# Kernel optimization log

Measured on AMD Instinct MI355X. Metric: run time of the kernel, lower is better.

The kernel has to match this reference:

```python
import jax, jax.numpy as jnp
import numpy as np

N_HEADS = 32
N_KV_HEADS = 8
HEAD_DIM = 64
ROPE_BASE = 10000.0


def _rope(t):
    # t: [b, s, h, d]; Llama-style rotate-half RoPE
    b, s, h, d = t.shape
    inv_freq = 1.0 / (ROPE_BASE ** (jnp.arange(0, d, 2, dtype=jnp.float32) / d))
    freqs = jnp.arange(s, dtype=jnp.float32)[:, None] * inv_freq[None, :]  # [s, d/2]
    cos = jnp.cos(freqs)[None, :, None, :].astype(t.dtype)
    sin = jnp.sin(freqs)[None, :, None, :].astype(t.dtype)
    t1, t2 = t[..., : d // 2], t[..., d // 2 :]
    return jnp.concatenate([t1 * cos - t2 * sin, t2 * cos + t1 * sin], axis=-1)


def setup_inputs() -> dict:
    key = jax.random.key(0)
    ks = jax.random.split(key, 5)
    b, s, d = 2, 2048, 2048
    dkv = d // (N_HEADS // N_KV_HEADS)
    sc = 1.0 / np.sqrt(d)
    return {
        "x": jax.random.normal(ks[0], (b, s, d), jnp.float32),
        "wq": jax.random.normal(ks[1], (d, d), jnp.float32) * sc,
        "wk": jax.random.normal(ks[2], (d, dkv), jnp.float32) * sc,
        "wv": jax.random.normal(ks[3], (d, dkv), jnp.float32) * sc,
        "wo": jax.random.normal(ks[4], (d, d), jnp.float32) * sc,
    }


def reference(x, wq, wk, wv, wo):
    b, s, d = x.shape
    g = N_HEADS // N_KV_HEADS
    q = (x @ wq).reshape(b, s, N_HEADS, HEAD_DIM)
    k = (x @ wk).reshape(b, s, N_KV_HEADS, HEAD_DIM)
    v = (x @ wv).reshape(b, s, N_KV_HEADS, HEAD_DIM)
    q = _rope(q)
    k = _rope(k)
    # GQA: repeat kv heads to match query heads
    k = jnp.repeat(k, g, axis=2)  # [b, s, N_HEADS, d_h]
    v = jnp.repeat(v, g, axis=2)
    scale = 1.0 / np.sqrt(HEAD_DIM)
    scores = jnp.einsum("bqhd,bkhd->bhqk", q, k) * scale  # [b, h, s, s]
    causal = jnp.tril(jnp.ones((s, s), dtype=bool))
    scores = jnp.where(causal[None, None], scores, jnp.finfo(scores.dtype).min)
    probs = jax.nn.softmax(scores, axis=-1)
    out = jnp.einsum("bhqk,bkhd->bqhd", probs, v).reshape(b, s, d)
    return out @ wo
```

## Files before the change

### kernel.cpp

```cpp
#include <hip/hip_runtime.h>
#include <hip/hip_bf16.h>
#include <stdint.h>

typedef __attribute__((ext_vector_type(8))) __bf16 bf16x8;
typedef __attribute__((ext_vector_type(4))) __bf16 bf16x4;
typedef __attribute__((ext_vector_type(4))) float f32x4;

#define QSCALE (0.125f * 1.44269504f)

#define GL16(src, dst) __builtin_amdgcn_global_load_lds( \
    (const __attribute__((address_space(1))) void*)(src), \
    (__attribute__((address_space(3))) void*)(dst), 16, 0, 0)

static __device__ inline unsigned pkbf(float a, float b) {
  __bf16 x = (__bf16)a, y = (__bf16)b;
  unsigned short ux = __builtin_bit_cast(unsigned short, x);
  unsigned short uy = __builtin_bit_cast(unsigned short, y);
  return ((unsigned)uy << 16) | ux;
}

static __device__ inline float ex2(float x) {
#if __has_builtin(__builtin_amdgcn_exp2f)
  return __builtin_amdgcn_exp2f(x);
#else
  float r;
  asm("v_exp_f32 %0, %1" : "=v"(r) : "v"(x));
  return r;
#endif
}

__global__ void k_cvt(const float* __restrict__ in, __bf16* __restrict__ out, int n8) {
  int i = blockIdx.x * blockDim.x + threadIdx.x;
  if (i >= n8) return;
  const float4* p = (const float4*)(in) + (size_t)i * 2;
  float4 a = p[0], b = p[1];
  bf16x8 o;
  o[0] = (__bf16)a.x; o[1] = (__bf16)a.y; o[2] = (__bf16)a.z; o[3] = (__bf16)a.w;
  o[4] = (__bf16)b.x; o[5] = (__bf16)b.y; o[6] = (__bf16)b.z; o[7] = (__bf16)b.w;
  ((bf16x8*)out)[i] = o;
}

__global__ void k_tconv(const float* __restrict__ w, __bf16* __restrict__ wT, int K, int N) {
  __shared__ float tile[32][33];
  int n0 = blockIdx.x * 32, k0 = blockIdx.y * 32;
  int tx = threadIdx.x, ty = threadIdx.y;
#pragma unroll
  for (int i = 0; i < 32; i += 8)
    tile[ty + i][tx] = w[(size_t)(k0 + ty + i) * N + n0 + tx];
  __syncthreads();
#pragma unroll
  for (int i = 0; i < 32; i += 8)
    wT[(size_t)(n0 + ty + i) * K + k0 + tx] = (__bf16)tile[tx][ty + i];
}

__global__ void k_ropetab(float* __restrict__ ct, float* __restrict__ st) {
  int i = blockIdx.x * blockDim.x + threadIdx.x;
  if (i >= 2048 * 32) return;
  int s = i >> 5, j = i & 31;
  float invf = powf(10000.0f, -(float)j / 32.0f);
  float fr = (float)s * invf;
  ct[i] = cosf(fr);
  st[i] = sinf(fr);
}

template <int BN, int NW, int WPN, int MODE>
__global__ __launch_bounds__(NW * 64, NW / 4) void k_gemm256(const __bf16* __restrict__ A,
                                                             const __bf16* __restrict__ BT,
                                                             void* __restrict__ C0,
                                                             __bf16* __restrict__ kb,
                                                             __bf16* __restrict__ vt,
                                                             const float* __restrict__ ct,
                                                             const float* __restrict__ st,
                                                             int K, int NBN) {
  constexpr int WPM = NW / WPN;
  constexpr int MF = 256 / WPM / 16;
  constexpr int NF = BN / WPN / 16;
  constexpr int MH = MF / 2;
  constexpr int CHA = 256 * 8;
  constexpr int CHB = BN * 8;
  constexpr int PA = CHA / (NW * 64);
  constexpr int RA = CHA - PA * NW * 64;
  constexpr int PB = CHB / (NW * 64);
  static_assert(CHB % (NW * 64) == 0, "B chunks must tile threads");
  static_assert(RA % 64 == 0, "A remainder must be wave-aligned");
  static_assert(NF == 4, "epilogue assumes 64-col wave window");
  __shared__ __align__(16) __bf16 lA[2][256 * 64];
  __shared__ __align__(16) __bf16 lB[2][BN * 64];
  int bm = (blockIdx.x / NBN) << 8;
  int bn = (blockIdx.x % NBN) * BN;
  int tid = threadIdx.x, l = tid & 63, w = tid >> 6;
  int wr = w / WPN, wc = w % WPN;
  int lrow = l & 15, lk = l >> 4;
  int NT = K >> 6;
  f32x4 acc[MF][NF] = {};

#define STG(T, BUF)                                                           \
  do {                                                                        \
    int k0_ = (T) << 6;                                                       \
    _Pragma("unroll") for (int i_ = 0; i_ < PA; i_++) {                       \
      int ch_ = i_ * (NW * 64) + tid;                                         \
      int r_ = ch_ >> 3, c_ = ch_ & 7;                                        \
      GL16(A + (size_t)(bm + r_) * K + k0_ + ((c_ ^ (r_ & 7)) << 3),          \
           &lA[BUF][(i_ * (NW * 64) + (w << 6)) * 8]);                        \
    }                                                                         \
    if constexpr (RA > 0) {                                                   \
      if (tid < RA) {                                                         \
        int ch_ = PA * (NW * 64) + tid;                                       \
        int r_ = ch_ >> 3, c_ = ch_ & 7;                                      \
        GL16(A + (size_t)(bm + r_) * K + k0_ + ((c_ ^ (r_ & 7)) << 3),        \
             &lA[BUF][(PA * (NW * 64) + (w << 6)) * 8]);                      \
      }                                                                       \
    }                                                                         \
    _Pragma("unroll") for (int i_ = 0; i_ < PB; i_++) {                       \
      int ch_ = i_ * (NW * 64) + tid;                                         \
      int r_ = ch_ >> 3, c_ = ch_ & 7;                                        \
      GL16(BT + (size_t)(bn + r_) * K + k0_ + ((c_ ^ (r_ & 7)) << 3),         \
           &lB[BUF][(i_ * (NW * 64) + (w << 6)) * 8]);                        \
    }                                                                         \
  } while (0)

#define WAITN()                                                               \
  do {                                                                        \
    if constexpr (RA > 0) {                                                   \
      if (w < (RA >> 6))                                                      \
        asm volatile("s_waitcnt vmcnt(%0)" ::"i"(PA + PB + 1) : "memory");    \
      else                                                                    \
        asm volatile("s_waitcnt vmcnt(%0)" ::"i"(PA + PB) : "memory");        \
    } else {                                                                  \
      asm volatile("s_waitcnt vmcnt(%0)" ::"i"(PA + PB) : "memory");          \
    }                                                                         \
  } while (0)

  STG(0, 0);
  STG(1, 1);
  WAITN();
  __builtin_amdgcn_sched_barrier(0);
  __builtin_amdgcn_s_barrier();

  for (int t = 0; t < NT; t++) {
    int buf = t & 1;
    const char* bA = (const char*)lA[buf];
    const char* bB = (const char*)lB[buf];
    bf16x8 bfr[NF][2], af0[MH][2], af1[MH][2];
#pragma unroll
    for (int nf = 0; nf < NF; nf++) {
      int row = wc * (NF * 16) + nf * 16 + lrow;
#pragma unroll
      for (int kc = 0; kc < 2; kc++)
        bfr[nf][kc] = *(const bf16x8*)(bB + row * 128 +
                                       ((kc * 64 + 16 * lk) ^ ((row & 7) << 4)));
    }
#pragma unroll
    for (int mf = 0; mf < MH; mf++) {
      int row = wr * (MF * 16) + mf * 16 + lrow;
#pragma unroll
      for (int kc = 0; kc < 2; kc++)
        af0[mf][kc] = *(const bf16x8*)(bA + row * 128 +
                                       ((kc * 64 + 16 * lk) ^ ((row & 7) << 4)));
    }
    __builtin_amdgcn_s_setprio(1);
#pragma unroll
    for (int kc = 0; kc < 2; kc++)
#pragma unroll
      for (int mf = 0; mf < MH; mf++)
#pragma unroll
        for (int nf = 0; nf < NF; nf++)
          acc[mf][nf] = __builtin_amdgcn_mfma_f32_16x16x32_bf16(af0[mf][kc], bfr[nf][kc],
                                                                acc[mf][nf], 0, 0, 0);
    __builtin_amdgcn_s_setprio(0);
#pragma unroll
    for (int mf = 0; mf < MH; mf++) {
      int row = wr * (MF * 16) + (MH + mf) * 16 + lrow;
#pragma unroll
      for (int kc = 0; kc < 2; kc++)
        af1[mf][kc] = *(const bf16x8*)(bA + row * 128 +
                                       ((kc * 64 + 16 * lk) ^ ((row & 7) << 4)));
    }
    asm volatile("s_waitcnt lgkmcnt(0)" ::: "memory");
    __builtin_amdgcn_sched_barrier(0);
    __builtin_amdgcn_s_barrier();
    if (t + 2 < NT) STG(t + 2, buf);
    __builtin_amdgcn_s_setprio(1);
#pragma unroll
    for (int kc = 0; kc < 2; kc++)
#pragma unroll
      for (int mf = 0; mf < MH; mf++)
#pragma unroll
        for (int nf = 0; nf < NF; nf++)
          acc[MH + mf][nf] = __builtin_amdgcn_mfma_f32_16x16x32_bf16(
              af1[mf][kc], bfr[nf][kc], acc[MH + mf][nf], 0, 0, 0);
    __builtin_amdgcn_s_setprio(0);
    if (t + 2 < NT) {
      WAITN();
    } else {
      asm volatile("s_waitcnt vmcnt(0)" ::: "memory");
    }
    __builtin_amdgcn_sched_barrier(0);
    __builtin_amdgcn_s_barrier();
  }
#undef STG
#undef WAITN

  if constexpr (MODE == 0) {
    int wcb = bn + wc * 64;
    __bf16* qb = (__bf16*)C0;
    if (wcb < 2048) {
#pragma unroll
      for (int mf = 0; mf < MF; mf++)
#pragma unroll
        for (int r = 0; r < 4; r++) {
          int row = bm + wr * (MF * 16) + mf * 16 + 4 * lk + r;
          int sidx = row & 2047;
#pragma unroll
          for (int nfl = 0; nfl < 2; nfl++) {
            int d = nfl * 16 + lrow;
            float c = ct[sidx * 32 + d], sn = st[sidx * 32 + d];
            float a = acc[mf][nfl][r], b2 = acc[mf][nfl + 2][r];
            qb[(size_t)row * 2048 + wcb + d] = (__bf16)((a * c - b2 * sn) * QSCALE);
            qb[(size_t)row * 2048 + wcb + d + 32] = (__bf16)((b2 * c + a * sn) * QSCALE);
          }
        }
    } else if (wcb < 2560) {
      int cb = wcb - 2048;
#pragma unroll
      for (int mf = 0; mf < MF; mf++)
#pragma unroll
        for (int r = 0; r < 4; r++) {
          int row = bm + wr * (MF * 16) + mf * 16 + 4 * lk + r;
          int sidx = row & 2047;
#pragma unroll
          for (int nfl = 0; nfl < 2; nfl++) {
            int d = nfl * 16 + lrow;
            float c = ct[sidx * 32 + d], sn = st[sidx * 32 + d];
            float a = acc[mf][nfl][r], b2 = acc[mf][nfl + 2][r];
            kb[(size_t)row * 512 + cb + d] = (__bf16)(a * c - b2 * sn);
            kb[(size_t)row * 512 + cb + d + 32] = (__bf16)(b2 * c + a * sn);
          }
        }
    } else {
      int hkk = (wcb - 2560) >> 6;
#pragma unroll
      for (int mf = 0; mf < MF; mf++)
#pragma unroll
        for (int nf = 0; nf < NF; nf++)
#pragma unroll
          for (int r = 0; r < 4; r++) {
            int row = bm + wr * (MF * 16) + mf * 16 + 4 * lk + r;
            int dd = nf * 16 + lrow;
            int bb = row >> 11, s = row & 2047;
            vt[(size_t)(((bb << 3) + hkk) * 64 + dd) * 2048 + s] = (__bf16)acc[mf][nf][r];
          }
    }
  } else {
    float* C = (float*)C0;
#pragma unroll
    for (int mf = 0; mf < MF; mf++)
#pragma unroll
      for (int nf = 0; nf < NF; nf++)
#pragma unroll
        for (int r = 0; r < 4; r++) {
          int row = bm + wr * (MF * 16) + mf * 16 + 4 * lk + r;
          int col = bn + wc * 64 + nf * 16 + lrow;
          C[(size_t)row * 2048 + col] = acc[mf][nf][r];
        }
  }
}

template <int BN, int NW, int WPN, int MODE>
__global__ __launch_bounds__(NW * 64, NW / 4) void k_gemm3d(const __bf16* __restrict__ A,
                                                            const __bf16* __restrict__ BT,
                                                            void* __restrict__ C0,
                                                            int K, int NBN) {
  constexpr int WPM = NW / WPN;
  constexpr int MF = 256 / WPM / 16;
  constexpr int NF = BN / WPN / 16;
  constexpr int MH = MF / 2;
  constexpr int CHA = 256 * 8;
  constexpr int CHB = BN * 8;
  constexpr int PA = CHA / (NW * 64);
  constexpr int RA = CHA - PA * NW * 64;
  constexpr int PB = CHB / (NW * 64);
  static_assert(CHB % (NW * 64) == 0, "B chunks must tile threads");
  static_assert(RA % 64 == 0, "A remainder must be wave-aligned");
  static_assert(NF == 4, "wave owns a 64-col window");
  constexpr int LB = PB;
  constexpr int LA0 = PA + (RA > 0 ? 1 : 0);
  constexpr int LA1 = PA;
  constexpr int NS0 = 2 * LA0 + LB, NS1 = 2 * LA1 + LB;
  constexpr int NM0 = LA0 + LB, NM1 = LA1 + LB;
  __shared__ __align__(16) __bf16 lA[3][256 * 64];
  __shared__ __align__(16) __bf16 lB[2][BN * 64];
  int bid = blockIdx.x;
  int lg = (bid & 7) * ((int)gridDim.x >> 3) + (bid >> 3);
  int bm = (lg / NBN) << 8;
  int bn = (lg % NBN) * BN;
  int tid = threadIdx.x, l = tid & 63, w = tid >> 6;
  int wr = w / WPN, wc = w % WPN;
  int lrow = l & 15, lk = l >> 4;
  int NT = K >> 6;
  f32x4 acc[MF][NF] = {};

#define STGA(T, BUF)                                                          \
  do {                                                                        \
    int k0_ = (T) << 6;                                                       \
    _Pragma("unroll") for (int i_ = 0; i_ < PA; i_++) {                       \
      int ch_ = i_ * (NW * 64) + tid;                                         \
      int r_ = ch_ >> 3, c_ = ch_ & 7;                                        \
      GL16(A + (size_t)(bm + r_) * K + k0_ + ((c_ ^ (r_ & 7)) << 3),          \
           &lA[BUF][(i_ * (NW * 64) + (w << 6)) * 8]);                        \
    }                                                                         \
    if constexpr (RA > 0) {                                                   \
      if (tid < RA) {                                                         \
        int ch_ = PA * (NW * 64) + tid;                                       \
        int r_ = ch_ >> 3, c_ = ch_ & 7;                                      \
        GL16(A + (size_t)(bm + r_) * K + k0_ + ((c_ ^ (r_ & 7)) << 3),        \
             &lA[BUF][(PA * (NW * 64) + (w << 6)) * 8]);                      \
      }                                                                       \
    }                                                                         \
  } while (0)

#define STGB(T, BUF)                                                          \
  do {                                                                        \
    int k0_ = (T) << 6;                                                       \
    _Pragma("unroll") for (int i_ = 0; i_ < PB; i_++) {                       \
      int ch_ = i_ * (NW * 64) + tid;                                         \
      int r_ = ch_ >> 3, c_ = ch_ & 7;                                        \
      GL16(BT + (size_t)(bn + r_) * K + k0_ + ((c_ ^ (r_ & 7)) << 3),         \
           &lB[BUF][(i_ * (NW * 64) + (w << 6)) * 8]);                        \
    }                                                                         \
  } while (0)

#define WAIT_STEADY()                                                         \
  do {                                                                        \
    if constexpr (RA > 0) {                                                   \
      if (w < (RA >> 6))                                                      \
        asm volatile("s_waitcnt vmcnt(%0)" ::"i"(NS0) : "memory");            \
      else                                                                    \
        asm volatile("s_waitcnt vmcnt(%0)" ::"i"(NS1) : "memory");            \
    } else {                                                                  \
      asm volatile("s_waitcnt vmcnt(%0)" ::"i"(NS1) : "memory");              \
    }                                                                         \
  } while (0)

#define WAIT_MID()                                                            \
  do {                                                                        \
    if constexpr (RA > 0) {                                                   \
      if (w < (RA >> 6))                                                      \
        asm volatile("s_waitcnt vmcnt(%0)" ::"i"(NM0) : "memory");            \
      else                                                                    \
        asm volatile("s_waitcnt vmcnt(%0)" ::"i"(NM1) : "memory");            \
    } else {                                                                  \
      asm volatile("s_waitcnt vmcnt(%0)" ::"i"(NM1) : "memory");              \
    }                                                                         \
  } while (0)

  STGB(0, 0); STGA(0, 0);
  STGB(1, 1); STGA(1, 1);
  STGA(2, 2);
  WAIT_STEADY();
  __builtin_amdgcn_sched_barrier(0);
  __builtin_amdgcn_s_barrier();

  int a0 = 0;
  for (int t = 0; t < NT; t++) {
    const char* bA = (const char*)lA[a0];
    const char* bB = (const char*)lB[t & 1];
    bf16x8 bfr[NF][2], af0[MH][2], af1[MH][2];
#pragma unroll
    for (int nf = 0; nf < NF; nf++) {
      int row = wc * (NF * 16) + nf * 16 + lrow;
#pragma unroll
      for (int kc = 0; kc < 2; kc++)
        bfr[nf][kc] = *(const bf16x8*)(bB + row * 128 +
                                       ((kc * 64 + 16 * lk) ^ ((row & 7) << 4)));
    }
#pragma unroll
    for (int mf = 0; mf < MH; mf++) {
      int row = wr * (MF * 16) + mf * 16 + lrow;
#pragma unroll
      for (int kc = 0; kc < 2; kc++)
        af0[mf][kc] = *(const bf16x8*)(bA + row * 128 +
                                       ((kc * 64 + 16 * lk) ^ ((row & 7) << 4)));
    }
#pragma unroll
    for (int mf = 0; mf < MH; mf++) {
      int row = wr * (MF * 16) + (MH + mf) * 16 + lrow;
#pragma unroll
      for (int kc = 0; kc < 2; kc++)
        af1[mf][kc] = *(const bf16x8*)(bA + row * 128 +
                                       ((kc * 64 + 16 * lk) ^ ((row & 7) << 4)));
    }
    __builtin_amdgcn_s_setprio(1);
#pragma unroll
    for (int kc = 0; kc < 2; kc++)
#pragma unroll
      for (int mf = 0; mf < MH; mf++)
#pragma unroll
        for (int nf = 0; nf < NF; nf++)
          acc[mf][nf] = __builtin_amdgcn_mfma_f32_16x16x32_bf16(af0[mf][kc], bfr[nf][kc],
                                                                acc[mf][nf], 0, 0, 0);
    __builtin_amdgcn_s_setprio(0);
    asm volatile("s_waitcnt lgkmcnt(0)" ::: "memory");
    __builtin_amdgcn_sched_barrier(0);
    __builtin_amdgcn_s_barrier();
    if (t + 2 < NT) STGB(t + 2, t & 1);
    if (t + 3 < NT) STGA(t + 3, a0);
    __builtin_amdgcn_s_setprio(1);
#pragma unroll
    for (int kc = 0; kc < 2; kc++)
#pragma unroll
      for (int mf = 0; mf < MH; mf++)
#pragma unroll
        for (int nf = 0; nf < NF; nf++)
          acc[MH + mf][nf] = __builtin_amdgcn_mfma_f32_16x16x32_bf16(
              af1[mf][kc], bfr[nf][kc], acc[MH + mf][nf], 0, 0, 0);
    __builtin_amdgcn_s_setprio(0);
    if (t + 3 < NT) {
      WAIT_STEADY();
    } else if (t + 2 < NT) {
      WAIT_MID();
    } else if (t + 1 < NT) {
      asm volatile("s_waitcnt vmcnt(0)" ::: "memory");
    }
    __builtin_amdgcn_sched_barrier(0);
    __builtin_amdgcn_s_barrier();
    a0 = (a0 == 2) ? 0 : a0 + 1;
  }
#undef STGA
#undef STGB
#undef WAIT_STEADY
#undef WAIT_MID

  float* C = (float*)C0;
#pragma unroll
  for (int mf = 0; mf < MF; mf++)
#pragma unroll
    for (int nf = 0; nf < NF; nf++)
#pragma unroll
      for (int r = 0; r < 4; r++) {
        int row = bm + wr * (MF * 16) + mf * 16 + 4 * lk + r;
        int col = bn + wc * 64 + nf * 16 + lrow;
        C[(size_t)row * 2048 + col] = acc[mf][nf][r];
      }
}

__global__ __launch_bounds__(256, 3) void k_attn(const __bf16* __restrict__ Q,
                                                 const __bf16* __restrict__ Kb,
                                                 const __bf16* __restrict__ VT,
                                                 __bf16* __restrict__ O) {
  __shared__ __align__(16) __bf16 lK[2][64 * 64];
  __shared__ __align__(16) __bf16 lV[2][64 * 64];
  int bid = blockIdx.x;
  int c = 63 - (bid >> 4);
  int hk = bid & 7;
  int b = (bid >> 3) & 1;
  int tid = threadIdx.x, l = tid & 63, w = tid >> 6;
  int h = hk * 4 + w;
  int lrow = l & 15, lk = l >> 4;
  int sw = (lrow & 7) << 4;
  int tl = c >> 1;

#define STAGE(BUF, T)                                                                     \
  do {                                                                                    \
    int kv0_ = (T) * 64;                                                                  \
    _Pragma("unroll") for (int i_ = 0; i_ < 2; i_++) {                                    \
      int cb_ = i_ * 256 + w * 64;                                                        \
      int chunk_ = cb_ + l;                                                               \
      int row_ = chunk_ >> 3, cc_ = chunk_ & 7;                                           \
      GL16(Kb + (size_t)(b * 2048 + kv0_ + row_) * 512 + hk * 64 +                        \
               ((cc_ ^ (row_ & 7)) << 3),                                                 \
           &lK[BUF][cb_ * 8]);                                                            \
      GL16(VT + (size_t)((b * 8 + hk) * 64 + row_) * 2048 + kv0_ +                        \
               ((cc_ ^ (row_ & 7)) << 3),                                                 \
           &lV[BUF][cb_ * 8]);                                                            \
    }                                                                                     \
  } while (0)

  bf16x8 aq[2][2];
#pragma unroll
  for (int qf = 0; qf < 2; qf++) {
    int qrow = c * 32 + qf * 16 + lrow;
    const __bf16* qp = Q + (size_t)(b * 2048 + qrow) * 2048 + h * 64 + lk * 8;
    aq[qf][0] = *(const bf16x8*)qp;
    aq[qf][1] = *(const bf16x8*)(qp + 32);
  }
  f32x4 o[2][4] = {};
  float lp[2] = {0.f, 0.f};
  STAGE(0, 0);
  for (int t = 0, buf = 0; t <= tl; t++, buf ^= 1) {
    asm volatile("s_waitcnt vmcnt(0)" ::: "memory");
    __syncthreads();
    if (t < tl) STAGE(buf ^ 1, t + 1);
    const char* K_ = (const char*)lK[buf];
    const char* V_ = (const char*)lV[buf];
    f32x4 s4[2][4];
    __builtin_amdgcn_s_setprio(1);
#pragma unroll
    for (int nf = 0; nf < 4; nf++) {
      const char* kr = K_ + (nf * 16 + lrow) * 128;
      bf16x8 bk0 = *(const bf16x8*)(kr + ((16 * lk) ^ sw));
      bf16x8 bk1 = *(const bf16x8*)(kr + ((64 + 16 * lk) ^ sw));
#pragma unroll
      for (int qf = 0; qf < 2; qf++) {
        f32x4 z = {};
        z = __builtin_amdgcn_mfma_f32_16x16x32_bf16(bk0, aq[qf][0], z, 0, 0, 0);
        z = __builtin_amdgcn_mfma_f32_16x16x32_bf16(bk1, aq[qf][1], z, 0, 0, 0);
        s4[qf][nf] = z;
      }
    }
    __builtin_amdgcn_s_setprio(0);
    if (t == tl) {
      int qo = (c & 1) * 32;
#pragma unroll
      for (int qf = 0; qf < 2; qf++) {
        int qoff = qo + qf * 16 + lrow;
#pragma unroll
        for (int nf = 0; nf < 4; nf++)
#pragma unroll
          for (int r = 0; r < 4; r++)
            if (nf * 16 + 4 * lk + r > qoff) s4[qf][nf][r] = -1e30f;
      }
    }
#pragma unroll
    for (int qf = 0; qf < 2; qf++) {
      float ps = 0.f;
#pragma unroll
      for (int nf = 0; nf < 4; nf++)
#pragma unroll
        for (int r = 0; r < 4; r++) {
          float pv = ex2(s4[qf][nf][r]);
          s4[qf][nf][r] = pv;
          ps += pv;
        }
      lp[qf] += ps;
    }
    __builtin_amdgcn_s_setprio(1);
#pragma unroll
    for (int np = 0; np < 2; np++) {
      bf16x8 pb[2];
#pragma unroll
      for (int qf = 0; qf < 2; qf++) {
        uint4 t4;
        t4.x = pkbf(s4[qf][np][0], s4[qf][np][1]);
        t4.y = pkbf(s4[qf][np][2], s4[qf][np][3]);
        t4.z = pkbf(s4[qf][np + 2][0], s4[qf][np + 2][1]);
        t4.w = pkbf(s4[qf][np + 2][2], s4[qf][np + 2][3]);
        pb[qf] = __builtin_bit_cast(bf16x8, t4);
      }
#pragma unroll
      for (int dn = 0; dn < 4; dn++) {
        const char* vr = V_ + (dn * 16 + lrow) * 128;
        uint2 a0 = *(const uint2*)(vr + ((np * 32 + 8 * lk) ^ sw));
        uint2 a1 = *(const uint2*)(vr + (((np + 2) * 32 + 8 * lk) ^ sw));
        uint4 av;
        av.x = a0.x; av.y = a0.y; av.z = a1.x; av.w = a1.y;
        bf16x8 va = __builtin_bit_cast(bf16x8, av);
#pragma unroll
        for (int qf = 0; qf < 2; qf++)
          o[qf][dn] = __builtin_amdgcn_mfma_f32_16x16x32_bf16(va, pb[qf], o[qf][dn], 0, 0, 0);
      }
    }
    __builtin_amdgcn_s_setprio(0);
  }
#pragma unroll
  for (int qf = 0; qf < 2; qf++) {
    float s = lp[qf];
    s += __shfl_xor(s, 16);
    s += __shfl_xor(s, 32);
    float inv = 1.f / s;
    int qrow = c * 32 + qf * 16 + lrow;
    __bf16* op = O + (size_t)(b * 2048 + qrow) * 2048 + h * 64 + 4 * lk;
#pragma unroll
    for (int dn = 0; dn < 4; dn++) {
      bf16x4 stv;
#pragma unroll
      for (int r = 0; r < 4; r++) stv[r] = (__bf16)(o[qf][dn][r] * inv);
      *(bf16x4*)(op + dn * 16) = stv;
    }
  }
#undef STAGE
}

extern "C" void kernel_launch(void* const* d_in, const int* in_sizes, int n_in,
                              void* d_out, int out_size, void* d_ws, size_t ws_size,
                              hipStream_t stream) {
  const float* x = (const float*)d_in[0];
  const float* wq = (const float*)d_in[1];
  const float* wk = (const float*)d_in[2];
  const float* wv = (const float*)d_in[3];
  const float* wo = (const float*)d_in[4];
  char* ws = (char*)d_ws;
  __bf16* xb    = (__bf16*)(ws + 0);
  __bf16* wqkvT = (__bf16*)(ws + 16777216);
  __bf16* woT   = (__bf16*)(ws + 29360128);
  __bf16* qb    = (__bf16*)(ws + 37748736);
  __bf16* kb    = (__bf16*)(ws + 54525952);
  __bf16* vt    = (__bf16*)(ws + 58720256);
  __bf16* ob    = (__bf16*)(ws + 62914560);
  float*  ct    = (float*)(ws + 79691776);
  float*  st    = (float*)(ws + 79953920);
  float* out = (float*)d_out;

  k_cvt<<<4096, 256, 0, stream>>>(x, xb, 1048576);
  k_tconv<<<dim3(64, 64), dim3(32, 8), 0, stream>>>(wq, wqkvT, 2048, 2048);
  k_tconv<<<dim3(16, 64), dim3(32, 8), 0, stream>>>(wk, wqkvT + (size_t)2048 * 2048, 2048, 512);
  k_tconv<<<dim3(16, 64), dim3(32, 8), 0, stream>>>(wv, wqkvT + (size_t)2560 * 2048, 2048, 512);
  k_tconv<<<dim3(64, 64), dim3(32, 8), 0, stream>>>(wo, woT, 2048, 2048);
  k_ropetab<<<256, 256, 0, stream>>>(ct, st);
  k_gemm256<192, 12, 3, 0><<<256, 768, 0, stream>>>(xb, wqkvT, qb, kb, vt, ct, st, 2048, 16);
  k_attn<<<1024, 256, 0, stream>>>(qb, kb, vt, ob);
  k_gemm3d<128, 8, 2, 1><<<256, 512, 0, stream>>>(ob, woT, out, 2048, 16);
}
```

Before: 168.4 us.

## Fuse prep kernels into one launch and rebalance causal attention block order

Merges the x conversion, the four weight transpose-converts and the RoPE table kernel into a single k_prep launch that dispatches on block index, removing five kernel launches and the idle gaps between them. Separately, attention blocks are reordered into four groups that interleave long and short causal chunks (descending, ascending, descending, ascending) instead of strictly longest-first, aiming for better load balance across waves. The merged kernel makes every block reserve the shared-memory transpose tile, and the new attention ordering may hurt tail behaviour compared with longest-first.

```diff
diff --git a/kernel.cpp b/kernel.cpp
--- a/kernel.cpp
+++ b/kernel.cpp
@@ -29,38 +29,54 @@
 #endif
 }
 
-__global__ void k_cvt(const float* __restrict__ in, __bf16* __restrict__ out, int n8) {
-  int i = blockIdx.x * blockDim.x + threadIdx.x;
-  if (i >= n8) return;
-  const float4* p = (const float4*)(in) + (size_t)i * 2;
-  float4 a = p[0], b = p[1];
-  bf16x8 o;
-  o[0] = (__bf16)a.x; o[1] = (__bf16)a.y; o[2] = (__bf16)a.z; o[3] = (__bf16)a.w;
-  o[4] = (__bf16)b.x; o[5] = (__bf16)b.y; o[6] = (__bf16)b.z; o[7] = (__bf16)b.w;
-  ((bf16x8*)out)[i] = o;
-}
-
-__global__ void k_tconv(const float* __restrict__ w, __bf16* __restrict__ wT, int K, int N) {
+__global__ __launch_bounds__(256) void k_prep(const float* __restrict__ x,
+                                              __bf16* __restrict__ xb,
+                                              const float* __restrict__ wq,
+                                              const float* __restrict__ wk,
+                                              const float* __restrict__ wv,
+                                              const float* __restrict__ wo,
+                                              __bf16* __restrict__ wqkvT,
+                                              __bf16* __restrict__ woT,
+                                              float* __restrict__ ct,
+                                              float* __restrict__ st) {
+  int bid = blockIdx.x, tid = threadIdx.x;
+  if (bid < 4096) {
+    int i = bid * 256 + tid;
+    const float4* p = (const float4*)(x) + (size_t)i * 2;
+    float4 a = p[0], b = p[1];
+    bf16x8 o;
+    o[0] = (__bf16)a.x; o[1] = (__bf16)a.y; o[2] = (__bf16)a.z; o[3] = (__bf16)a.w;
+    o[4] = (__bf16)b.x; o[5] = (__bf16)b.y; o[6] = (__bf16)b.z; o[7] = (__bf16)b.w;
+    ((bf16x8*)xb)[i] = o;
+    return;
+  }
+  if (bid >= 14336) {
+    int i = (bid - 14336) * 256 + tid;
+    int s = i >> 5, j = i & 31;
+    float invf = powf(10000.0f, -(float)j / 32.0f);
+    float fr = (float)s * invf;
+    ct[i] = cosf(fr);
+    st[i] = sinf(fr);
+    return;
+  }
   __shared__ float tile[32][33];
-  int n0 = blockIdx.x * 32, k0 = blockIdx.y * 32;
-  int tx = threadIdx.x, ty = threadIdx.y;
+  const float* w;
+  __bf16* wT;
+  int N, r;
+  if (bid < 8192)       { r = bid - 4096;  w = wq; wT = wqkvT;                        N = 2048; }
+  else if (bid < 9216)  { r = bid - 8192;  w = wk; wT = wqkvT + (size_t)2048 * 2048;  N = 512; }
+  else if (bid < 10240) { r = bid - 9216;  w = wv; wT = wqkvT + (size_t)2560 * 2048;  N = 512; }
+  else                  { r = bid - 10240; w = wo; wT = woT;                          N = 2048; }
+  int ntiles = N >> 5;
+  int n0 = (r % ntiles) * 32, k0 = (r / ntiles) * 32;
+  int tx = tid & 31, ty = tid >> 5;
 #pragma unroll
   for (int i = 0; i < 32; i += 8)
     tile[ty + i][tx] = w[(size_t)(k0 + ty + i) * N + n0 + tx];
   __syncthreads();
 #pragma unroll
   for (int i = 0; i < 32; i += 8)
-    wT[(size_t)(n0 + ty + i) * K + k0 + tx] = (__bf16)tile[tx][ty + i];
-}
-
-__global__ void k_ropetab(float* __restrict__ ct, float* __restrict__ st) {
-  int i = blockIdx.x * blockDim.x + threadIdx.x;
-  if (i >= 2048 * 32) return;
-  int s = i >> 5, j = i & 31;
-  float invf = powf(10000.0f, -(float)j / 32.0f);
-  float fr = (float)s * invf;
-  ct[i] = cosf(fr);
-  st[i] = sinf(fr);
+    wT[(size_t)(n0 + ty + i) * 2048 + k0 + tx] = (__bf16)tile[tx][ty + i];
 }
 
 template <int BN, int NW, int WPN, int MODE>
@@ -451,7 +467,12 @@
   __shared__ __align__(16) __bf16 lK[2][64 * 64];
   __shared__ __align__(16) __bf16 lV[2][64 * 64];
   int bid = blockIdx.x;
-  int c = 63 - (bid >> 4);
+  int g = bid >> 8, k = (bid >> 4) & 15;
+  int c;
+  if (g == 0) c = 63 - k;
+  else if (g == 1) c = 32 + k;
+  else if (g == 2) c = 31 - k;
+  else c = k;
   int hk = bid & 7;
   int b = (bid >> 3) & 1;
   int tid = threadIdx.x, l = tid & 63, w = tid >> 6;
@@ -601,12 +622,7 @@
   float*  st    = (float*)(ws + 79953920);
   float* out = (float*)d_out;
 
-  k_cvt<<<4096, 256, 0, stream>>>(x, xb, 1048576);
-  k_tconv<<<dim3(64, 64), dim3(32, 8), 0, stream>>>(wq, wqkvT, 2048, 2048);
-  k_tconv<<<dim3(16, 64), dim3(32, 8), 0, stream>>>(wk, wqkvT + (size_t)2048 * 2048, 2048, 512);
-  k_tconv<<<dim3(16, 64), dim3(32, 8), 0, stream>>>(wv, wqkvT + (size_t)2560 * 2048, 2048, 512);
-  k_tconv<<<dim3(64, 64), dim3(32, 8), 0, stream>>>(wo, woT, 2048, 2048);
-  k_ropetab<<<256, 256, 0, stream>>>(ct, st);
+  k_prep<<<14592, 256, 0, stream>>>(x, xb, wq, wk, wv, wo, wqkvT, woT, ct, st);
   k_gemm256<192, 12, 3, 0><<<256, 768, 0, stream>>>(xb, wqkvT, qb, kb, vt, ct, st, 2048, 16);
   k_attn<<<1024, 256, 0, stream>>>(qb, kb, vt, ob);
   k_gemm3d<128, 8, 2, 1><<<256, 512, 0, stream>>>(ob, woT, out, 2048, 16);
```

Result: faster. 162.3 us (-3.6%).
